# Performance work log

Measured on AMD Instinct MI355X. Metric: run time of the kernel, lower is better.

Reference implementation:

```python
import jax, jax.numpy as jnp
import numpy as np

BS = 16384   # batch size
D = 2048     # input_dim
BD = 64      # block_dim
NB = D // BD # 32 blocks per BlockMLP
H = 2 * BD   # hidden block dim (hidden_layers_ratio=[2])
NUM_LAYERS = 2  # ceil(log_64(2048)) = 2


def setup_inputs() -> dict:
    key = jax.random.key(0)
    ks = jax.random.split(key, 1 + 2 * NUM_LAYERS)
    inp = {"x": jax.random.normal(ks[0], (BS, D), dtype=jnp.float32)}
    for i in range(NUM_LAYERS):
        inp[f"W1_{i}"] = jax.random.normal(ks[1 + 2 * i], (NB, BD, H), dtype=jnp.float32)
        inp[f"b1_{i}"] = jnp.zeros((NB, 1, H), dtype=jnp.float32)
        inp[f"W2_{i}"] = jax.random.normal(ks[2 + 2 * i], (NB, H, BD), dtype=jnp.float32)
        inp[f"b2_{i}"] = jnp.zeros((NB, 1, BD), dtype=jnp.float32)
    return inp


def _block_mlp(y, W1, b1, W2, b2):
    # BlockMLP.forward: view(bs, n_blocks, block_dim) -> transpose to [n_blocks, bs, block_dim]
    bs = y.shape[0]
    yb = y.reshape(bs, NB, BD).transpose(1, 0, 2)          # [NB, bs, BD]
    h = jnp.einsum('nbi,nio->nbo', yb, W1) + b1             # [NB, bs, H]
    h = jax.nn.gelu(h, approximate=False)                   # torch nn.GELU default (erf)
    o = jnp.einsum('nbh,nho->nbo', h, W2) + b2              # [NB, bs, BD]
    return o.transpose(1, 0, 2).reshape(bs, -1)             # [bs, D]


def reference(x, W1_0, b1_0, W2_0, b2_0, W1_1, b1_1, W2_1, b2_1):
    bs = x.shape[0]
    params = [(W1_0, b1_0, W2_0, b2_0), (W1_1, b1_1, W2_1, b2_1)]
    y = x
    for i, (W1, b1, W2, b2) in enumerate(params):
        # butterfly-style mixing permute before the block MLP
        y = y.reshape(-1, BD, BD ** i).transpose(0, 2, 1).reshape(bs, -1)
        y = _block_mlp(y, W1, b1, W2, b2)
        # inverse-style permute after
        y = y.reshape(-1, BD ** i, BD).transpose(0, 2, 1)
    return y.reshape(bs, -1)
```

## Files before the change

### kernel.cpp

```cpp
#include <hip/hip_runtime.h>

#define D    2048
#define NB   32
#define BD   64
#define HD   128
#define WSZ  (NB * HD * BD)
#define TSZ  (16384 * 64)

typedef __attribute__((ext_vector_type(8))) short short8;
typedef __attribute__((ext_vector_type(4))) float floatx4;

static __device__ __forceinline__ unsigned short f2bf(float f) {
  union { float f; unsigned u; } v; v.f = f;
  return (unsigned short)((v.u + 0x7FFFu + ((v.u >> 16) & 1u)) >> 16);
}
static __device__ __forceinline__ float bf2f(unsigned short h) {
  union { unsigned u; float f; } v; v.u = ((unsigned)h) << 16;
  return v.f;
}
static __device__ __forceinline__ unsigned fbits(float f) {
  union { float f; unsigned u; } v; v.f = f; return v.u;
}
static __device__ __forceinline__ unsigned pkt(float a, float b) {
  return __builtin_amdgcn_perm(fbits(b), fbits(a), 0x07060302u);
}
static __device__ __forceinline__ float fast_exp2(float x) {
  float r; asm("v_exp_f32 %0, %1" : "=v"(r) : "v"(x)); return r;
}
static __device__ __forceinline__ float fast_rcp(float x) {
  float r; asm("v_rcp_f32 %0, %1" : "=v"(r) : "v"(x)); return r;
}
static __device__ __forceinline__ float gelu_f(float x) {
  float x2 = x * x;
  float w  = __builtin_fmaf(x2, -0.102943695f, -2.3022083f);
  float e  = fast_exp2(x * w);
  return x * fast_rcp(1.0f + e);
}

template<bool F32IN>
__global__ __launch_bounds__(256, 4) void mlp_layer(
    const float* __restrict__ xf,
    unsigned short* yio,
    const unsigned short* __restrict__ Wt1,
    const unsigned short* __restrict__ Wt2,
    const float* __restrict__ b1,
    const float* __restrict__ b2) {
  __shared__ unsigned short Wlds[16384];
  __shared__ float Blds[192];
  const int n     = blockIdx.x & 31;
  const int chunk = blockIdx.x >> 5;
  const int t = threadIdx.x, l = t & 63, wv = t >> 6;
  const int lr = l & 15, q = l >> 4;
  const int sw = (lr & 7) << 3;
  const int rbase = chunk * 128 + wv * 32 + lr;

  const unsigned short* s1 = Wt1 + n * 8192;
  const unsigned short* s2 = Wt2 + n * 8192;
  short8 sv1[4], sv2[4];
#pragma unroll
  for (int j = 0; j < 4; ++j) {
    sv1[j] = *(const short8*)&s1[(j * 256 + t) * 8];
    sv2[j] = *(const short8*)&s2[(j * 256 + t) * 8];
  }
  float bv = 0.f;
  if (t < 128)      bv = b1[n * HD + t];
  else if (t < 192) bv = b2[n * BD + (t - 128)];

  float4 uf[2][4];
  short8 xp[2][2];
  if constexpr (F32IN) {
#pragma unroll
    for (int p = 0; p < 2; ++p) {
      const float* xr = xf + (size_t)(rbase + p * 16) * D + n * BD + q * 8;
      uf[p][0] = *(const float4*)(xr);      uf[p][1] = *(const float4*)(xr + 4);
      uf[p][2] = *(const float4*)(xr + 32); uf[p][3] = *(const float4*)(xr + 36);
    }
  } else {
#pragma unroll
    for (int p = 0; p < 2; ++p) {
      const unsigned short* yr = yio + (size_t)n * TSZ + (size_t)(rbase + p * 16) * 64 + q * 8;
      xp[p][0] = *(const short8*)(yr); xp[p][1] = *(const short8*)(yr + 32);
    }
  }

  asm volatile("" ::: "memory");

#pragma unroll
  for (int j = 0; j < 4; ++j) {
    *(short8*)&Wlds[(j * 256 + t) * 8]        = sv1[j];
    *(short8*)&Wlds[8192 + (j * 256 + t) * 8] = sv2[j];
  }
  if (t < 192) Blds[t] = bv;

  __syncthreads();

  const unsigned short* w1p0 = &Wlds[lr * 64 + ((q * 8) ^ sw)];
  const unsigned short* w1p1 = &Wlds[lr * 64 + ((32 + q * 8) ^ sw)];
  const unsigned short* w2p0 = &Wlds[8192 + lr * 128 + ((q * 8) ^ sw)];
  const unsigned short* w2p1 = &Wlds[8192 + lr * 128 + ((32 + q * 8) ^ sw)];

#pragma unroll
  for (int i = 0; i < 2; ++i) {
    short8 xb0, xb1;
    if constexpr (F32IN) {
      union { unsigned u[4]; short8 s; } c0, c1;
      c0.u[0] = pkt(uf[i][0].x, uf[i][0].y);
      c0.u[1] = pkt(uf[i][0].z, uf[i][0].w);
      c0.u[2] = pkt(uf[i][1].x, uf[i][1].y);
      c0.u[3] = pkt(uf[i][1].z, uf[i][1].w);
      c1.u[0] = pkt(uf[i][2].x, uf[i][2].y);
      c1.u[1] = pkt(uf[i][2].z, uf[i][2].w);
      c1.u[2] = pkt(uf[i][3].x, uf[i][3].y);
      c1.u[3] = pkt(uf[i][3].z, uf[i][3].w);
      xb0 = c0.s; xb1 = c1.s;
    } else {
      xb0 = xp[i][0]; xb1 = xp[i][1];
    }

    floatx4 acc2[4];
#pragma unroll
    for (int ot = 0; ot < 4; ++ot) {
      const float4 bb = *(const float4*)&Blds[128 + ot * 16 + q * 4];
      floatx4 v; v[0] = bb.x; v[1] = bb.y; v[2] = bb.z; v[3] = bb.w;
      acc2[ot] = v;
    }
#pragma unroll
    for (int hf = 0; hf < 2; ++hf) {
      floatx4 acc1[4];
#pragma unroll
      for (int ot = 0; ot < 4; ++ot) {
        const float4 bb = *(const float4*)&Blds[hf * 64 + ot * 16 + q * 4];
        floatx4 v; v[0] = bb.x; v[1] = bb.y; v[2] = bb.z; v[3] = bb.w;
        acc1[ot] = v;
      }
#pragma unroll
      for (int ot = 0; ot < 4; ++ot) {
        const int off = (hf * 64 + ot * 16) * 64;
        short8 a0 = *(const short8*)&w1p0[off];
        short8 a1 = *(const short8*)&w1p1[off];
        acc1[ot] = __builtin_amdgcn_mfma_f32_16x16x32_bf16(a0, xb0, acc1[ot], 0, 0, 0);
        acc1[ot] = __builtin_amdgcn_mfma_f32_16x16x32_bf16(a1, xb1, acc1[ot], 0, 0, 0);
      }
      union { unsigned u[4]; short8 s; } hb0, hb1;
      hb0.u[0] = pkt(gelu_f(acc1[0][0]), gelu_f(acc1[0][1]));
      hb0.u[1] = pkt(gelu_f(acc1[0][2]), gelu_f(acc1[0][3]));
      hb0.u[2] = pkt(gelu_f(acc1[1][0]), gelu_f(acc1[1][1]));
      hb0.u[3] = pkt(gelu_f(acc1[1][2]), gelu_f(acc1[1][3]));
      hb1.u[0] = pkt(gelu_f(acc1[2][0]), gelu_f(acc1[2][1]));
      hb1.u[1] = pkt(gelu_f(acc1[2][2]), gelu_f(acc1[2][3]));
      hb1.u[2] = pkt(gelu_f(acc1[3][0]), gelu_f(acc1[3][1]));
      hb1.u[3] = pkt(gelu_f(acc1[3][2]), gelu_f(acc1[3][3]));
#pragma unroll
      for (int ot = 0; ot < 4; ++ot) {
        const int off = ot * 16 * 128 + hf * 64;
        short8 w0 = *(const short8*)&w2p0[off];
        short8 w1 = *(const short8*)&w2p1[off];
        acc2[ot] = __builtin_amdgcn_mfma_f32_16x16x32_bf16(w0, hb0.s, acc2[ot], 0, 0, 0);
        acc2[ot] = __builtin_amdgcn_mfma_f32_16x16x32_bf16(w1, hb1.s, acc2[ot], 0, 0, 0);
      }
    }

    unsigned short* yo = yio + (size_t)n * TSZ + (size_t)(rbase + i * 16) * 64;
#pragma unroll
    for (int ot = 0; ot < 4; ++ot) {
      if constexpr (F32IN) {
        uint2 ov;
        ov.x = pkt(acc2[ot][0], acc2[ot][1]);
        ov.y = pkt(acc2[ot][2], acc2[ot][3]);
        *(uint2*)&yo[ot * 16 + q * 4] = ov;
      } else {
        ushort4 ov;
        ov.x = f2bf(acc2[ot][0]);
        ov.y = f2bf(acc2[ot][1]);
        ov.z = f2bf(acc2[ot][2]);
        ov.w = f2bf(acc2[ot][3]);
        *(ushort4*)&yo[ot * 16 + q * 4] = ov;
      }
    }
  }
}

__global__ __launch_bounds__(256) void permute_k(unsigned short* Y) {
  __shared__ unsigned short L[32 * 512];
  const int t = threadIdx.x, w = t >> 6, j = t & 63;
  const size_t r0 = (size_t)blockIdx.x * 8;
#pragma unroll
  for (int c = 0; c < 8; ++c) {
    const int n = w * 8 + c;
    short8 v = *(const short8*)(Y + (size_t)n * TSZ + r0 * 64 + j * 8);
    const int row = j >> 3;
    const int gp = (j & 7) ^ ((n + row) & 7);
    *(short8*)&L[n * 512 + row * 64 + gp * 8] = v;
  }
  __syncthreads();
#pragma unroll
  for (int c = 0; c < 8; ++c) {
    const int np  = w * 8 + c;
    const int row = j >> 3;
    short8 o;
#pragma unroll
    for (int k = 0; k < 8; ++k) {
      const int fp   = (j & 7) * 8 + k;
      const int n    = fp & 31;
      const int srow = (row & ~1) | (fp >> 5);
      const int scol = (row & 1) * 32 + np;
      const int g    = ((scol >> 3) ^ ((n + srow) & 7));
      o[k] = (short)L[n * 512 + srow * 64 + g * 8 + (scol & 7)];
    }
    *(short8*)(Y + (size_t)np * TSZ + r0 * 64 + j * 8) = o;
  }
}

__global__ __launch_bounds__(256) void unpermute_k(const unsigned short* __restrict__ Y,
                                                   float* __restrict__ out) {
  __shared__ unsigned short L[32 * 512];
  const int t = threadIdx.x, w = t >> 6, j = t & 63;
  const size_t r0 = (size_t)blockIdx.x * 8;
#pragma unroll
  for (int c = 0; c < 8; ++c) {
    const int n = w * 8 + c;
    short8 v = *(const short8*)(Y + (size_t)n * TSZ + r0 * 64 + j * 8);
    const int row = j >> 3;
    const int gp = (j & 7) ^ ((n + row) & 7);
    *(short8*)&L[n * 512 + row * 64 + gp * 8] = v;
  }
  __syncthreads();
#pragma unroll
  for (int p = 0; p < 2; ++p) {
    const int rloc = w * 2 + p;
    float* op = out + (r0 + rloc) * (size_t)D;
#pragma unroll
    for (int i = 0; i < 8; ++i) {
      const int cbase = i * 256 + j * 4;
      float4 f;
#pragma unroll
      for (int e = 0; e < 4; ++e) {
        const int cc   = cbase + e;
        const int np   = cc >> 6, fp = cc & 63;
        const int n    = fp & 31;
        const int srow = (rloc & ~1) | (fp >> 5);
        const int scol = (rloc & 1) * 32 + np;
        const int g    = ((scol >> 3) ^ ((n + srow) & 7));
        const float v  = bf2f(L[n * 512 + srow * 64 + g * 8 + (scol & 7)]);
        if      (e == 0) f.x = v;
        else if (e == 1) f.y = v;
        else if (e == 2) f.z = v;
        else             f.w = v;
      }
      *(float4*)&op[cbase] = f;
    }
  }
}

__global__ void prep_w_all(const float* __restrict__ W1_0, const float* __restrict__ W2_0,
                           const float* __restrict__ W1_1, const float* __restrict__ W2_1,
                           unsigned short* __restrict__ dst) {
  const int seg = blockIdx.x >> 10;
  const int id  = ((blockIdx.x & 1023) << 8) | threadIdx.x;
  const float* W; int R;
  if      (seg == 0) { W = W1_0; R = BD; }
  else if (seg == 1) { W = W2_0; R = HD; }
  else if (seg == 2) { W = W1_1; R = BD; }
  else               { W = W2_1; R = HD; }
  const int C   = (R == BD) ? HD : BD;
  const int n   = id >> 13;
  const int rem = id & 8191;
  const int c   = rem / R;
  const int r   = rem - c * R;
  const unsigned short val = f2bf(W[(n * R + r) * C + c]);
  if (seg & 1) {
    const int hf  = r >> 6, st = (r >> 5) & 1, blk = (r >> 4) & 1;
    const int qq  = (r & 15) >> 2, e = r & 3;
    const int slot = hf * 64 + st * 32 + qq * 8 + blk * 4 + e;
    dst[seg * WSZ + n * 8192 + c * HD + (slot ^ ((c & 7) << 3))] = val;
  } else {
    dst[seg * WSZ + n * 8192 + c * BD + (r ^ ((c & 7) << 3))] = val;
  }
}

extern "C" void kernel_launch(void* const* d_in, const int* in_sizes, int n_in,
                              void* d_out, int out_size, void* d_ws, size_t ws_size,
                              hipStream_t stream) {
  const float* x    = (const float*)d_in[0];
  const float* W1_0 = (const float*)d_in[1];
  const float* b1_0 = (const float*)d_in[2];
  const float* W2_0 = (const float*)d_in[3];
  const float* b2_0 = (const float*)d_in[4];
  const float* W1_1 = (const float*)d_in[5];
  const float* b1_1 = (const float*)d_in[6];
  const float* W2_1 = (const float*)d_in[7];
  const float* b2_1 = (const float*)d_in[8];
  float* out = (float*)d_out;

  unsigned short* Wt = (unsigned short*)d_ws;
  unsigned short* Yt = Wt + 4 * WSZ;

  prep_w_all<<<4096, 256, 0, stream>>>(W1_0, W2_0, W1_1, W2_1, Wt);
  mlp_layer<true ><<<4096, 256, 0, stream>>>(x, Yt, Wt, Wt + WSZ, b1_0, b2_0);
  permute_k<<<2048, 256, 0, stream>>>(Yt);
  mlp_layer<false><<<4096, 256, 0, stream>>>(nullptr, Yt, Wt + 2 * WSZ, Wt + 3 * WSZ, b1_1, b2_1);
  unpermute_k<<<2048, 256, 0, stream>>>(Yt, out);
}
```

Measured before the change: 171.9 us.

## Fuse inter-layer permute into MLP kernels via LDS transposes

Removes the standalone permute kernel. The first MLP kernel now stages its outputs in LDS and writes them in a transposed, feature-major layout. The second MLP kernel gathers its inputs from that layout through an LDS transpose. This saves one full read and write pass over the bf16 intermediate and one kernel launch. In exchange it adds LDS use, which is why launch bounds drop from 4 to 3 blocks per CU. It also switches layer-0 output rounding to truncation and adds a second intermediate buffer.

```diff
diff --git a/kernel.cpp b/kernel.cpp
--- a/kernel.cpp
+++ b/kernel.cpp
@@ -21,6 +21,9 @@
 static __device__ __forceinline__ unsigned fbits(float f) {
   union { float f; unsigned u; } v; v.f = f; return v.u;
 }
+static __device__ __forceinline__ unsigned short tbf(float f) {
+  return (unsigned short)(fbits(f) >> 16);
+}
 static __device__ __forceinline__ unsigned pkt(float a, float b) {
   return __builtin_amdgcn_perm(fbits(b), fbits(a), 0x07060302u);
 }
@@ -37,15 +40,14 @@
   return x * fast_rcp(1.0f + e);
 }
 
-template<bool F32IN>
-__global__ __launch_bounds__(256, 4) void mlp_layer(
+__global__ __launch_bounds__(256, 3) void mlp0_k(
     const float* __restrict__ xf,
-    unsigned short* yio,
+    unsigned short* __restrict__ Yt0,
     const unsigned short* __restrict__ Wt1,
     const unsigned short* __restrict__ Wt2,
-    const float* __restrict__ b1,
-    const float* __restrict__ b2) {
+    const float* __restrict__ b1, const float* __restrict__ b2) {
   __shared__ unsigned short Wlds[16384];
+  __shared__ unsigned short Olds[64 * 128];
   __shared__ float Blds[192];
   const int n     = blockIdx.x & 31;
   const int chunk = blockIdx.x >> 5;
@@ -65,33 +67,20 @@
   float bv = 0.f;
   if (t < 128)      bv = b1[n * HD + t];
   else if (t < 192) bv = b2[n * BD + (t - 128)];
-
   float4 uf[2][4];
-  short8 xp[2][2];
-  if constexpr (F32IN) {
-#pragma unroll
-    for (int p = 0; p < 2; ++p) {
-      const float* xr = xf + (size_t)(rbase + p * 16) * D + n * BD + q * 8;
-      uf[p][0] = *(const float4*)(xr);      uf[p][1] = *(const float4*)(xr + 4);
-      uf[p][2] = *(const float4*)(xr + 32); uf[p][3] = *(const float4*)(xr + 36);
-    }
-  } else {
-#pragma unroll
-    for (int p = 0; p < 2; ++p) {
-      const unsigned short* yr = yio + (size_t)n * TSZ + (size_t)(rbase + p * 16) * 64 + q * 8;
-      xp[p][0] = *(const short8*)(yr); xp[p][1] = *(const short8*)(yr + 32);
-    }
-  }
-
+#pragma unroll
+  for (int p = 0; p < 2; ++p) {
+    const float* xr = xf + (size_t)(rbase + p * 16) * D + n * BD + q * 8;
+    uf[p][0] = *(const float4*)(xr);      uf[p][1] = *(const float4*)(xr + 4);
+    uf[p][2] = *(const float4*)(xr + 32); uf[p][3] = *(const float4*)(xr + 36);
+  }
   asm volatile("" ::: "memory");
-
 #pragma unroll
   for (int j = 0; j < 4; ++j) {
     *(short8*)&Wlds[(j * 256 + t) * 8]        = sv1[j];
     *(short8*)&Wlds[8192 + (j * 256 + t) * 8] = sv2[j];
   }
   if (t < 192) Blds[t] = bv;
-
   __syncthreads();
 
   const unsigned short* w1p0 = &Wlds[lr * 64 + ((q * 8) ^ sw)];
@@ -102,7 +91,7 @@
 #pragma unroll
   for (int i = 0; i < 2; ++i) {
     short8 xb0, xb1;
-    if constexpr (F32IN) {
+    {
       union { unsigned u[4]; short8 s; } c0, c1;
       c0.u[0] = pkt(uf[i][0].x, uf[i][0].y);
       c0.u[1] = pkt(uf[i][0].z, uf[i][0].w);
@@ -113,10 +102,7 @@
       c1.u[2] = pkt(uf[i][3].x, uf[i][3].y);
       c1.u[3] = pkt(uf[i][3].z, uf[i][3].w);
       xb0 = c0.s; xb1 = c1.s;
-    } else {
-      xb0 = xp[i][0]; xb1 = xp[i][1];
-    }
-
+    }
     floatx4 acc2[4];
 #pragma unroll
     for (int ot = 0; ot < 4; ++ot) {
@@ -159,28 +145,151 @@
         acc2[ot] = __builtin_amdgcn_mfma_f32_16x16x32_bf16(w1, hb1.s, acc2[ot], 0, 0, 0);
       }
     }
-
-    unsigned short* yo = yio + (size_t)n * TSZ + (size_t)(rbase + i * 16) * 64;
+    const int rl = wv * 32 + i * 16 + lr;
 #pragma unroll
     for (int ot = 0; ot < 4; ++ot) {
-      if constexpr (F32IN) {
-        uint2 ov;
-        ov.x = pkt(acc2[ot][0], acc2[ot][1]);
-        ov.y = pkt(acc2[ot][2], acc2[ot][3]);
-        *(uint2*)&yo[ot * 16 + q * 4] = ov;
-      } else {
-        ushort4 ov;
-        ov.x = f2bf(acc2[ot][0]);
-        ov.y = f2bf(acc2[ot][1]);
-        ov.z = f2bf(acc2[ot][2]);
-        ov.w = f2bf(acc2[ot][3]);
-        *(ushort4*)&yo[ot * 16 + q * 4] = ov;
-      }
-    }
-  }
-}
-
-__global__ __launch_bounds__(256) void permute_k(unsigned short* Y) {
+#pragma unroll
+      for (int e = 0; e < 4; ++e) {
+        const int fo = ot * 16 + q * 4 + e;
+        Olds[fo * 128 + (rl ^ ((fo & 7) << 3))] = tbf(acc2[ot][e]);
+      }
+    }
+  }
+  __syncthreads();
+
+  const int j = t & 63, w = t >> 6;
+#pragma unroll
+  for (int ii = 0; ii < 8; ++ii) {
+    const int fo = w * 16 + ii * 2 + (j >> 5);
+    const int r4 = (j & 31) * 4;
+    const int G  = (fo & 7) << 3;
+    uint2 v = *(const uint2*)&Olds[fo * 128 + (r4 ^ G)];
+    *(uint2*)(Yt0 + (size_t)n * TSZ + (size_t)fo * 16384 + chunk * 128 + r4) = v;
+  }
+}
+
+__global__ __launch_bounds__(256, 3) void mlp1_k(
+    const unsigned short* __restrict__ Yt0,
+    unsigned short* __restrict__ Yt1,
+    const unsigned short* __restrict__ Wt1,
+    const unsigned short* __restrict__ Wt2,
+    const float* __restrict__ b1, const float* __restrict__ b2) {
+  __shared__ unsigned short Wlds[16384];
+  __shared__ unsigned short Xl[2 * 128 * 32];
+  __shared__ float Blds[192];
+  const int np    = blockIdx.x & 31;
+  const int chunk = blockIdx.x >> 5;
+  const int t = threadIdx.x, l = t & 63, wv = t >> 6;
+  const int lr = l & 15, q = l >> 4;
+  const int sw = (lr & 7) << 3;
+
+  const unsigned short* s1 = Wt1 + np * 8192;
+  const unsigned short* s2 = Wt2 + np * 8192;
+  short8 sv1[4], sv2[4];
+#pragma unroll
+  for (int j = 0; j < 4; ++j) {
+    sv1[j] = *(const short8*)&s1[(j * 256 + t) * 8];
+    sv2[j] = *(const short8*)&s2[(j * 256 + t) * 8];
+  }
+  float bv = 0.f;
+  if (t < 128)      bv = b1[np * HD + t];
+  else if (t < 192) bv = b2[np * BD + (t - 128)];
+  const int c = t >> 2, sub = t & 3;
+  const int sp = c >> 5, sn = c & 31;
+  const unsigned short* src = Yt0 + (size_t)sn * TSZ + (size_t)(sp * 32 + np) * 16384
+                              + chunk * 128 + sub * 32;
+  short8 sx[4];
+#pragma unroll
+  for (int m = 0; m < 4; ++m) sx[m] = *(const short8*)(src + m * 8);
+
+  asm volatile("" ::: "memory");
+#pragma unroll
+  for (int j = 0; j < 4; ++j) {
+    *(short8*)&Wlds[(j * 256 + t) * 8]        = sv1[j];
+    *(short8*)&Wlds[8192 + (j * 256 + t) * 8] = sv2[j];
+  }
+  if (t < 192) Blds[t] = bv;
+#pragma unroll
+  for (int m = 0; m < 4; ++m) {
+#pragma unroll
+    for (int k = 0; k < 8; ++k) {
+      const int row = sub * 32 + m * 8 + k;
+      Xl[sp * 4096 + row * 32 + (sn ^ (((row >> 1) & 3) << 3))] = (unsigned short)sx[m][k];
+    }
+  }
+  __syncthreads();
+
+  const unsigned short* w1p0 = &Wlds[lr * 64 + ((q * 8) ^ sw)];
+  const unsigned short* w1p1 = &Wlds[lr * 64 + ((32 + q * 8) ^ sw)];
+  const unsigned short* w2p0 = &Wlds[8192 + lr * 128 + ((q * 8) ^ sw)];
+  const unsigned short* w2p1 = &Wlds[8192 + lr * 128 + ((32 + q * 8) ^ sw)];
+  const int p = lr & 1;
+
+#pragma unroll
+  for (int i = 0; i < 2; ++i) {
+    const int rloc = (wv * 32 + i * 16 + lr) & ~1;
+    const int g0   = ((rloc >> 1) & 3) << 3;
+    short8 xb0 = *(const short8*)&Xl[p * 4096 + rloc * 32 + ((q * 8) ^ g0)];
+    short8 xb1 = *(const short8*)&Xl[p * 4096 + (rloc + 1) * 32 + ((q * 8) ^ g0)];
+
+    floatx4 acc2[4];
+#pragma unroll
+    for (int ot = 0; ot < 4; ++ot) {
+      const float4 bb = *(const float4*)&Blds[128 + ot * 16 + q * 4];
+      floatx4 v; v[0] = bb.x; v[1] = bb.y; v[2] = bb.z; v[3] = bb.w;
+      acc2[ot] = v;
+    }
+#pragma unroll
+    for (int hf = 0; hf < 2; ++hf) {
+      floatx4 acc1[4];
+#pragma unroll
+      for (int ot = 0; ot < 4; ++ot) {
+        const float4 bb = *(const float4*)&Blds[hf * 64 + ot * 16 + q * 4];
+        floatx4 v; v[0] = bb.x; v[1] = bb.y; v[2] = bb.z; v[3] = bb.w;
+        acc1[ot] = v;
+      }
+#pragma unroll
+      for (int ot = 0; ot < 4; ++ot) {
+        const int off = (hf * 64 + ot * 16) * 64;
+        short8 a0 = *(const short8*)&w1p0[off];
+        short8 a1 = *(const short8*)&w1p1[off];
+        acc1[ot] = __builtin_amdgcn_mfma_f32_16x16x32_bf16(a0, xb0, acc1[ot], 0, 0, 0);
+        acc1[ot] = __builtin_amdgcn_mfma_f32_16x16x32_bf16(a1, xb1, acc1[ot], 0, 0, 0);
+      }
+      union { unsigned u[4]; short8 s; } hb0, hb1;
+      hb0.u[0] = pkt(gelu_f(acc1[0][0]), gelu_f(acc1[0][1]));
+      hb0.u[1] = pkt(gelu_f(acc1[0][2]), gelu_f(acc1[0][3]));
+      hb0.u[2] = pkt(gelu_f(acc1[1][0]), gelu_f(acc1[1][1]));
+      hb0.u[3] = pkt(gelu_f(acc1[1][2]), gelu_f(acc1[1][3]));
+      hb1.u[0] = pkt(gelu_f(acc1[2][0]), gelu_f(acc1[2][1]));
+      hb1.u[1] = pkt(gelu_f(acc1[2][2]), gelu_f(acc1[2][3]));
+      hb1.u[2] = pkt(gelu_f(acc1[3][0]), gelu_f(acc1[3][1]));
+      hb1.u[3] = pkt(gelu_f(acc1[3][2]), gelu_f(acc1[3][3]));
+#pragma unroll
+      for (int ot = 0; ot < 4; ++ot) {
+        const int off = ot * 16 * 128 + hf * 64;
+        short8 w0 = *(const short8*)&w2p0[off];
+        short8 w1 = *(const short8*)&w2p1[off];
+        acc2[ot] = __builtin_amdgcn_mfma_f32_16x16x32_bf16(w0, hb0.s, acc2[ot], 0, 0, 0);
+        acc2[ot] = __builtin_amdgcn_mfma_f32_16x16x32_bf16(w1, hb1.s, acc2[ot], 0, 0, 0);
+      }
+    }
+    unsigned short* yo = Yt1 + (size_t)np * TSZ
+                       + (size_t)(chunk * 128 + wv * 32 + i * 16 + lr) * 64;
+#pragma unroll
+    for (int ot = 0; ot < 4; ++ot) {
+      ushort4 ov;
+      ov.x = f2bf(acc2[ot][0]);
+      ov.y = f2bf(acc2[ot][1]);
+      ov.z = f2bf(acc2[ot][2]);
+      ov.w = f2bf(acc2[ot][3]);
+      *(ushort4*)&yo[ot * 16 + q * 4] = ov;
+    }
+  }
+}
+
+__global__ __launch_bounds__(256) void unpermute_k(const unsigned short* __restrict__ Y,
+                                                   float* __restrict__ out) {
   __shared__ unsigned short L[32 * 512];
   const int t = threadIdx.x, w = t >> 6, j = t & 63;
   const size_t r0 = (size_t)blockIdx.x * 8;
@@ -194,38 +303,6 @@
   }
   __syncthreads();
 #pragma unroll
-  for (int c = 0; c < 8; ++c) {
-    const int np  = w * 8 + c;
-    const int row = j >> 3;
-    short8 o;
-#pragma unroll
-    for (int k = 0; k < 8; ++k) {
-      const int fp   = (j & 7) * 8 + k;
-      const int n    = fp & 31;
-      const int srow = (row & ~1) | (fp >> 5);
-      const int scol = (row & 1) * 32 + np;
-      const int g    = ((scol >> 3) ^ ((n + srow) & 7));
-      o[k] = (short)L[n * 512 + srow * 64 + g * 8 + (scol & 7)];
-    }
-    *(short8*)(Y + (size_t)np * TSZ + r0 * 64 + j * 8) = o;
-  }
-}
-
-__global__ __launch_bounds__(256) void unpermute_k(const unsigned short* __restrict__ Y,
-                                                   float* __restrict__ out) {
-  __shared__ unsigned short L[32 * 512];
-  const int t = threadIdx.x, w = t >> 6, j = t & 63;
-  const size_t r0 = (size_t)blockIdx.x * 8;
-#pragma unroll
-  for (int c = 0; c < 8; ++c) {
-    const int n = w * 8 + c;
-    short8 v = *(const short8*)(Y + (size_t)n * TSZ + r0 * 64 + j * 8);
-    const int row = j >> 3;
-    const int gp = (j & 7) ^ ((n + row) & 7);
-    *(short8*)&L[n * 512 + row * 64 + gp * 8] = v;
-  }
-  __syncthreads();
-#pragma unroll
   for (int p = 0; p < 2; ++p) {
     const int rloc = w * 2 + p;
     float* op = out + (r0 + rloc) * (size_t)D;
@@ -236,10 +313,10 @@
 #pragma unroll
       for (int e = 0; e < 4; ++e) {
         const int cc   = cbase + e;
-        const int np   = cc >> 6, fp = cc & 63;
+        const int npp  = cc >> 6, fp = cc & 63;
         const int n    = fp & 31;
         const int srow = (rloc & ~1) | (fp >> 5);
-        const int scol = (rloc & 1) * 32 + np;
+        const int scol = (rloc & 1) * 32 + npp;
         const int g    = ((scol >> 3) ^ ((n + srow) & 7));
         const float v  = bf2f(L[n * 512 + srow * 64 + g * 8 + (scol & 7)]);
         if      (e == 0) f.x = v;
@@ -292,12 +369,12 @@
   const float* b2_1 = (const float*)d_in[8];
   float* out = (float*)d_out;
 
-  unsigned short* Wt = (unsigned short*)d_ws;
-  unsigned short* Yt = Wt + 4 * WSZ;
+  unsigned short* Wt  = (unsigned short*)d_ws;
+  unsigned short* Yt0 = Wt + 4 * WSZ;
+  unsigned short* Yt1 = Yt0 + (size_t)NB * TSZ;
 
   prep_w_all<<<4096, 256, 0, stream>>>(W1_0, W2_0, W1_1, W2_1, Wt);
-  mlp_layer<true ><<<4096, 256, 0, stream>>>(x, Yt, Wt, Wt + WSZ, b1_0, b2_0);
-  permute_k<<<2048, 256, 0, stream>>>(Yt);
-  mlp_layer<false><<<4096, 256, 0, stream>>>(nullptr, Yt, Wt + 2 * WSZ, Wt + 3 * WSZ, b1_1, b2_1);
-  unpermute_k<<<2048, 256, 0, stream>>>(Yt, out);
-}
+  mlp0_k<<<4096, 256, 0, stream>>>(x, Yt0, Wt, Wt + WSZ, b1_0, b2_0);
+  mlp1_k<<<4096, 256, 0, stream>>>(Yt0, Yt1, Wt + 2 * WSZ, Wt + 3 * WSZ, b1_1, b2_1);
+  unpermute_k<<<2048, 256, 0, stream>>>(Yt1, out);
+}
```

Result: faster. 140.6 us (-18.2%).
